# Kernel tuning notes

Measured on AMD Instinct MI355X. Metric: run time of the kernel, lower is better.

The kernel has to match this reference:

```python
import jax, jax.numpy as jnp
import numpy as np

N = 200000
H = W = 1024
C_IN, C_MID = 256, 64
EPS = 1e-6


def _build_neighbor_idx():
    # Sample N unique occupied sites on an HxW grid; build 3x3 kernel maps.
    rng = np.random.default_rng(0)
    perm = rng.permutation(H * W)[:N]
    grid = -np.ones(H * W, dtype=np.int64)
    grid[perm] = np.arange(N)
    ys, xs = perm // W, perm % W
    maps = []
    for dy in (-1, 0, 1):
        for dx in (-1, 0, 1):
            ny, nx = ys + dy, xs + dx
            valid = (ny >= 0) & (ny < H) & (nx >= 0) & (nx < W)
            lin = np.clip(ny * W + nx, 0, H * W - 1)
            nb = grid[lin]
            maps.append(np.where(valid & (nb >= 0), nb, N))  # sentinel N = missing
    return jnp.asarray(np.stack(maps).astype(np.int32))  # [9, N]


def setup_inputs() -> dict:
    key = jax.random.key(0)
    ks = jax.random.split(key, 4)
    return {
        "x": jax.random.normal(ks[0], (N, C_IN), jnp.float32),
        "W1": jax.random.normal(ks[1], (C_IN, C_MID), jnp.float32) * (C_IN ** -0.5),
        "W2": jax.random.normal(ks[2], (9, C_MID, C_MID), jnp.float32) * ((9 * C_MID) ** -0.5),
        "W3": jax.random.normal(ks[3], (C_MID, C_IN), jnp.float32) * (C_MID ** -0.5),
        "g1": jnp.ones((C_MID,), jnp.float32),
        "b1": jnp.zeros((C_MID,), jnp.float32),
        "g2": jnp.ones((C_MID,), jnp.float32),
        "b2": jnp.zeros((C_MID,), jnp.float32),
        "g3": jnp.ones((C_IN,), jnp.float32),
        "b3": jnp.zeros((C_IN,), jnp.float32),
        "neighbor_idx": _build_neighbor_idx(),
    }


def _ln(h, g, b):
    mu = jnp.mean(h, axis=-1, keepdims=True)
    var = jnp.mean(jnp.square(h - mu), axis=-1, keepdims=True)
    return (h - mu) * jax.lax.rsqrt(var + EPS) * g + b


def reference(x, W1, W2, W3, g1, b1, g2, b2, g3, b3, neighbor_idx):
    # conv1 (1x1 sparse conv == per-point linear) -> LN -> GELU
    h = jax.nn.gelu(_ln(x @ W1, g1, b1), approximate=False)
    # conv2: 3x3 sparse conv via gather-GEMM over kernel maps, sentinel row = zeros
    h_pad = jnp.concatenate([h, jnp.zeros((1, h.shape[1]), h.dtype)], axis=0)
    gathered = h_pad[neighbor_idx]               # [9, N, C_MID]
    h = jnp.einsum('knc,kcd->nd', gathered, W2)  # [N, C_MID]
    h = jax.nn.gelu(_ln(h, g2, b2), approximate=False)
    # conv3 (1x1) -> LN, residual, GELU
    h = _ln(h @ W3, g3, b3)
    return jax.nn.gelu(h + x, approximate=False)
```

## Files before the change

### kernel.cpp

```cpp
#include <hip/hip_runtime.h>
#include <math.h>

#define NPTS 200000
#define LNEPS 1e-6f

typedef unsigned short u16;
typedef __attribute__((ext_vector_type(4))) float  f4;
typedef __attribute__((ext_vector_type(8))) short  s8;

__device__ __forceinline__ u16 f2b(float f) {
    union { float f; unsigned u; } v; v.f = f;
    unsigned r = v.u + 0x7fffu + ((v.u >> 16) & 1u);
    return (u16)(r >> 16);
}

__device__ __forceinline__ float gelu_f(float v) {
    float u = v * (0.7978845608028654f + 0.035677408136300125f * v * v);
    u = fminf(u, 15.0f);
    float e = __builtin_amdgcn_exp2f(u * 2.8853900817779268f);
    return 0.5f * v * (1.0f + (e - 1.0f) * __builtin_amdgcn_rcpf(e + 1.0f));
}

__global__ __launch_bounds__(256) void k0_convw(
    const float* __restrict__ W1, const float* __restrict__ W2,
    const float* __restrict__ W3,
    u16* __restrict__ W1f, u16* __restrict__ W2f, u16* __restrict__ W3f,
    u16* __restrict__ h1)
{
    int t = blockIdx.x * 256 + threadIdx.x;
    if (t < 16384) {
        int j = t & 7, l = (t >> 3) & 63, ks = (t >> 9) & 7, nt = t >> 12;
        int k = 32 * ks + (l >> 4) * 8 + j;
        int n = 16 * nt + (l & 15);
        W1f[t] = f2b(W1[k * 64 + n]);
    }
    if (t < 36864) {
        int kk = t >> 12;
        int r = t & 4095;
        int j = r & 7, l = (r >> 3) & 63, ks = (r >> 9) & 1, nt = r >> 10;
        int k = 32 * ks + (l >> 4) * 8 + j;
        int n = 16 * nt + (l & 15);
        W2f[t] = f2b(W2[(kk * 64 + k) * 64 + n]);
    }
    if (t < 16384) {
        int j = t & 7, l = (t >> 3) & 63, ks = (t >> 9) & 1, nt = t >> 10;
        int k = 32 * ks + (l >> 4) * 8 + j;
        int n = 16 * nt + (l & 15);
        W3f[t] = f2b(W3[k * 256 + n]);
    }
    if (t < 64) h1[(long)NPTS * 64 + t] = 0;
}

__global__ __launch_bounds__(256) void k1_conv1(
    const float* __restrict__ x, const u16* __restrict__ W1f,
    const float* __restrict__ g1, const float* __restrict__ b1,
    u16* __restrict__ h1)
{
    int tid = threadIdx.x;
    int w = tid >> 6, l = tid & 63, lg = l >> 4, lr = l & 15;
    long base = (long)blockIdx.x * 64 + w * 16;
    const float* xrow = x + (base + lr) * 256;

    f4 xa[16];
    #pragma unroll
    for (int ks = 0; ks < 8; ++ks) {
        xa[2 * ks]     = *(const f4*)(xrow + 32 * ks + lg * 8);
        xa[2 * ks + 1] = *(const f4*)(xrow + 32 * ks + lg * 8 + 4);
    }

    f4 acc[4] = {};
    #pragma unroll
    for (int ks = 0; ks < 8; ++ks) {
        f4 a0 = xa[2 * ks], a1 = xa[2 * ks + 1];
        s8 a;
        a[0] = (short)f2b(a0[0]); a[1] = (short)f2b(a0[1]);
        a[2] = (short)f2b(a0[2]); a[3] = (short)f2b(a0[3]);
        a[4] = (short)f2b(a1[0]); a[5] = (short)f2b(a1[1]);
        a[6] = (short)f2b(a1[2]); a[7] = (short)f2b(a1[3]);
        #pragma unroll
        for (int nt = 0; nt < 4; ++nt) {
            s8 b = *(const s8*)(W1f + ((nt * 8 + ks) * 64 + l) * 8);
            acc[nt] = __builtin_amdgcn_mfma_f32_16x16x32_bf16(a, b, acc[nt], 0, 0, 0);
        }
    }

    #pragma unroll
    for (int r = 0; r < 4; ++r) {
        float sv = 0.f, qv = 0.f;
        #pragma unroll
        for (int nt = 0; nt < 4; ++nt) { float v = acc[nt][r]; sv += v; qv += v * v; }
        #pragma unroll
        for (int m = 1; m < 16; m <<= 1) { sv += __shfl_xor(sv, m); qv += __shfl_xor(qv, m); }
        float mu  = sv * (1.0f / 64.0f);
        float var = qv * (1.0f / 64.0f) - mu * mu;
        float rs  = rsqrtf(var + LNEPS);
        long row = base + lg * 4 + r;
        #pragma unroll
        for (int nt = 0; nt < 4; ++nt) {
            int col = 16 * nt + lr;
            float v = (acc[nt][r] - mu) * rs * g1[col] + b1[col];
            h1[row * 64 + col] = f2b(gelu_f(v));
        }
    }
}

__global__ __launch_bounds__(256) void k2_fused(
    const u16* __restrict__ h1, const u16* __restrict__ W2f,
    const u16* __restrict__ W3f, const float* __restrict__ x,
    const float* __restrict__ g2, const float* __restrict__ b2,
    const float* __restrict__ g3, const float* __restrict__ b3,
    const int* __restrict__ nidx, float* __restrict__ out)
{
    __shared__ __align__(16) u16 A3[4][16][72];
    int tid = threadIdx.x;
    int w = tid >> 6, l = tid & 63, lg = l >> 4, lr = l & 15;
    long base = (long)blockIdx.x * 64 + w * 16;
    long rowa = base + lr;

    int idxs[9];
    #pragma unroll
    for (int k = 0; k < 9; ++k) idxs[k] = nidx[(long)k * NPTS + rowa];

    s8 afr[9][2];
    #pragma unroll
    for (int k = 0; k < 9; ++k) {
        const u16* arow = h1 + (long)idxs[k] * 64;
        afr[k][0] = *(const s8*)(arow + lg * 8);
        afr[k][1] = *(const s8*)(arow + 32 + lg * 8);
    }

    f4 acc2[4] = {};
    #pragma unroll
    for (int k = 0; k < 9; ++k) {
        #pragma unroll
        for (int ks = 0; ks < 2; ++ks) {
            #pragma unroll
            for (int nt = 0; nt < 4; ++nt) {
                s8 b = *(const s8*)(W2f + (long)k * 4096 + ((nt * 2 + ks) * 64 + l) * 8);
                acc2[nt] = __builtin_amdgcn_mfma_f32_16x16x32_bf16(afr[k][ks], b, acc2[nt], 0, 0, 0);
            }
        }
    }

    #pragma unroll
    for (int r = 0; r < 4; ++r) {
        float sv = 0.f, qv = 0.f;
        #pragma unroll
        for (int nt = 0; nt < 4; ++nt) { float v = acc2[nt][r]; sv += v; qv += v * v; }
        #pragma unroll
        for (int m = 1; m < 16; m <<= 1) { sv += __shfl_xor(sv, m); qv += __shfl_xor(qv, m); }
        float mu  = sv * (1.0f / 64.0f);
        float var = qv * (1.0f / 64.0f) - mu * mu;
        float rs  = rsqrtf(var + LNEPS);
        #pragma unroll
        for (int nt = 0; nt < 4; ++nt) {
            int col = 16 * nt + lr;
            float v = (acc2[nt][r] - mu) * rs * g2[col] + b2[col];
            A3[w][lg * 4 + r][col] = f2b(gelu_f(v));
        }
    }
    __syncthreads();

    s8 a0 = *(const s8*)(&A3[w][lr][lg * 8]);
    s8 a1 = *(const s8*)(&A3[w][lr][32 + lg * 8]);
    f4 acc3[16] = {};
    #pragma unroll
    for (int nt = 0; nt < 16; ++nt) {
        s8 b0 = *(const s8*)(W3f + ((nt * 2 + 0) * 64 + l) * 8);
        s8 b1 = *(const s8*)(W3f + ((nt * 2 + 1) * 64 + l) * 8);
        acc3[nt] = __builtin_amdgcn_mfma_f32_16x16x32_bf16(a0, b0, acc3[nt], 0, 0, 0);
        acc3[nt] = __builtin_amdgcn_mfma_f32_16x16x32_bf16(a1, b1, acc3[nt], 0, 0, 0);
    }

    #pragma unroll
    for (int r = 0; r < 4; ++r) {
        float sv = 0.f, qv = 0.f;
        #pragma unroll
        for (int nt = 0; nt < 16; ++nt) { float v = acc3[nt][r]; sv += v; qv += v * v; }
        #pragma unroll
        for (int m = 1; m < 16; m <<= 1) { sv += __shfl_xor(sv, m); qv += __shfl_xor(qv, m); }
        float mu  = sv * (1.0f / 256.0f);
        float var = qv * (1.0f / 256.0f) - mu * mu;
        float rs  = rsqrtf(var + LNEPS);
        long row = base + lg * 4 + r;
        const float* xr = x + row * 256;
        float* outr = out + row * 256;
        #pragma unroll
        for (int nt = 0; nt < 16; ++nt) {
            int col = 16 * nt + lr;
            float v = (acc3[nt][r] - mu) * rs * g3[col] + b3[col];
            v += xr[col];
            outr[col] = gelu_f(v);
        }
    }
}

extern "C" void kernel_launch(void* const* d_in, const int* in_sizes, int n_in,
                              void* d_out, int out_size, void* d_ws, size_t ws_size,
                              hipStream_t stream)
{
    const float* x  = (const float*)d_in[0];
    const float* W1 = (const float*)d_in[1];
    const float* W2 = (const float*)d_in[2];
    const float* W3 = (const float*)d_in[3];
    const float* g1 = (const float*)d_in[4];
    const float* b1 = (const float*)d_in[5];
    const float* g2 = (const float*)d_in[6];
    const float* b2 = (const float*)d_in[7];
    const float* g3 = (const float*)d_in[8];
    const float* b3 = (const float*)d_in[9];
    const int* nidx = (const int*)d_in[10];
    float* out = (float*)d_out;

    char* ws = (char*)d_ws;
    u16* W1f = (u16*)(ws);
    u16* W2f = (u16*)(ws + 32768);
    u16* W3f = (u16*)(ws + 106496);
    u16* h1  = (u16*)(ws + 139264);

    hipLaunchKernelGGL(k0_convw, dim3(144), dim3(256), 0, stream,
                       W1, W2, W3, W1f, W2f, W3f, h1);
    hipLaunchKernelGGL(k1_conv1, dim3(3125), dim3(256), 0, stream,
                       x, W1f, g1, b1, h1);
    hipLaunchKernelGGL(k2_fused, dim3(3125), dim3(256), 0, stream,
                       h1, W2f, W3f, x, g2, b2, g3, b3, nidx, out);
}
```

Before: 214.6 us.

## Split fused conv2/conv3 kernel into two kernels with bf16 intermediate

Splits the fused gather-conv2 plus conv3 kernel into two kernels connected by a bf16 h2 buffer in workspace, and adds launch-bounds occupancy hints of four blocks. Each kernel then needs fewer registers (the 9x2 gathered fragments and the 16 conv3 accumulators are no longer live in the same kernel), and the LDS buffer and barrier go away, which should raise occupancy and latency hiding for the gather. In exchange it adds a 25.6 MB write and read of h2 plus an extra kernel launch.

Measured after the change: 220.2 us. 2.6% more time.

```diff
diff --git a/kernel.cpp b/kernel.cpp
--- a/kernel.cpp
+++ b/kernel.cpp
@@ -104,14 +104,11 @@
     }
 }
 
-__global__ __launch_bounds__(256) void k2_fused(
+__global__ __launch_bounds__(256, 4) void k2a_conv2(
     const u16* __restrict__ h1, const u16* __restrict__ W2f,
-    const u16* __restrict__ W3f, const float* __restrict__ x,
     const float* __restrict__ g2, const float* __restrict__ b2,
-    const float* __restrict__ g3, const float* __restrict__ b3,
-    const int* __restrict__ nidx, float* __restrict__ out)
-{
-    __shared__ __align__(16) u16 A3[4][16][72];
+    const int* __restrict__ nidx, u16* __restrict__ h2)
+{
     int tid = threadIdx.x;
     int w = tid >> 6, l = tid & 63, lg = l >> 4, lr = l & 15;
     long base = (long)blockIdx.x * 64 + w * 16;
@@ -152,17 +149,30 @@
         float mu  = sv * (1.0f / 64.0f);
         float var = qv * (1.0f / 64.0f) - mu * mu;
         float rs  = rsqrtf(var + LNEPS);
+        long row = base + lg * 4 + r;
         #pragma unroll
         for (int nt = 0; nt < 4; ++nt) {
             int col = 16 * nt + lr;
             float v = (acc2[nt][r] - mu) * rs * g2[col] + b2[col];
-            A3[w][lg * 4 + r][col] = f2b(gelu_f(v));
-        }
-    }
-    __syncthreads();
-
-    s8 a0 = *(const s8*)(&A3[w][lr][lg * 8]);
-    s8 a1 = *(const s8*)(&A3[w][lr][32 + lg * 8]);
+            h2[row * 64 + col] = f2b(gelu_f(v));
+        }
+    }
+}
+
+__global__ __launch_bounds__(256, 4) void k2b_conv3(
+    const u16* __restrict__ h2, const u16* __restrict__ W3f,
+    const float* __restrict__ x,
+    const float* __restrict__ g3, const float* __restrict__ b3,
+    float* __restrict__ out)
+{
+    int tid = threadIdx.x;
+    int w = tid >> 6, l = tid & 63, lg = l >> 4, lr = l & 15;
+    long base = (long)blockIdx.x * 64 + w * 16;
+
+    const u16* arow = h2 + (base + lr) * 64;
+    s8 a0 = *(const s8*)(arow + lg * 8);
+    s8 a1 = *(const s8*)(arow + 32 + lg * 8);
+
     f4 acc3[16] = {};
     #pragma unroll
     for (int nt = 0; nt < 16; ++nt) {
@@ -217,11 +227,14 @@
     u16* W2f = (u16*)(ws + 32768);
     u16* W3f = (u16*)(ws + 106496);
     u16* h1  = (u16*)(ws + 139264);
+    u16* h2  = (u16*)(ws + 139264 + 25600128);
 
     hipLaunchKernelGGL(k0_convw, dim3(144), dim3(256), 0, stream,
                        W1, W2, W3, W1f, W2f, W3f, h1);
     hipLaunchKernelGGL(k1_conv1, dim3(3125), dim3(256), 0, stream,
                        x, W1f, g1, b1, h1);
-    hipLaunchKernelGGL(k2_fused, dim3(3125), dim3(256), 0, stream,
-                       h1, W2f, W3f, x, g2, b2, g3, b3, nidx, out);
-}
+    hipLaunchKernelGGL(k2a_conv2, dim3(3125), dim3(256), 0, stream,
+                       h1, W2f, g2, b2, nidx, h2);
+    hipLaunchKernelGGL(k2b_conv3, dim3(3125), dim3(256), 0, stream,
+                       h2, W3f, x, g3, b3, out);
+}
```
